# Optimization experiments

Hardware: AMD Instinct MI355X
Metric: run time of the kernel (lower is better)

Reference implementation:

```python
import jax, jax.numpy as jnp
import numpy as np

N = 100000
E = 3200000
H_MLP = 30   # EdgeMLP hidden dim
H_GCN = 10   # GCNEvaluator hidden dim
D_IN = 6     # node_dim + token_dim


def setup_inputs() -> dict:
    key = jax.random.key(0)
    ks = jax.random.split(key, 24)
    s = 0.1
    inp = {
        "x": jax.random.normal(ks[0], (N, 1), jnp.float32),
        "token": jax.random.normal(ks[1], (N, 5), jnp.float32),
        "edge_attr_gen": jax.random.normal(ks[2], (E, 1), jnp.float32),
        "edge_attr_eval": jax.random.uniform(ks[3], (E, 2), jnp.float32),
        "gumbel": jax.random.gumbel(ks[4], (E, 2), jnp.float32),
        "edge_index": jax.random.randint(ks[5], (2, E), 0, N, jnp.int32),
        # EdgeMLP params: Linear(13,30), Linear(30,30), Linear(30,30), Linear(30,2)
        "W0": jax.random.normal(ks[6], (2 * D_IN + 1, H_MLP), jnp.float32) * s,
        "b0": jnp.zeros((H_MLP,), jnp.float32),
        "W1": jax.random.normal(ks[7], (H_MLP, H_MLP), jnp.float32) * s,
        "b1": jnp.zeros((H_MLP,), jnp.float32),
        "W2": jax.random.normal(ks[8], (H_MLP, H_MLP), jnp.float32) * s,
        "b2": jnp.zeros((H_MLP,), jnp.float32),
        "W3": jax.random.normal(ks[9], (H_MLP, 2), jnp.float32) * s,
        "b3": jnp.zeros((2,), jnp.float32),
        # GCNEvaluator params
        "Wl": jax.random.normal(ks[10], (1, 1), jnp.float32) * s,   # edge_weight_lin
        "bl": jnp.zeros((1,), jnp.float32),
        "Wc": jax.random.normal(ks[11], (D_IN, H_GCN), jnp.float32) * s,  # GCNConv weight
        "bc": jnp.zeros((H_GCN,), jnp.float32),
        "Wo": jax.random.normal(ks[12], (H_GCN, 1), jnp.float32) * s,     # output Linear
        "bo": jnp.zeros((1,), jnp.float32),
    }
    return inp


def reference(x, token, edge_attr_gen, edge_attr_eval, gumbel, edge_index,
              W0, b0, W1, b1, W2, b2, W3, b3, Wl, bl, Wc, bc, Wo, bo):
    src = edge_index[0]
    tgt = edge_index[1]
    x_all = jnp.concatenate([x, token], axis=-1)              # [N, 6]

    # ---- generate_graph: edge gather + concat + MLP ----
    ef = jnp.concatenate([x_all[src], x_all[tgt], edge_attr_gen], axis=-1)  # [E, 13]
    h = jax.nn.relu(ef @ W0 + b0)
    h = jax.nn.relu(h @ W1 + b1)
    h = jax.nn.relu(h @ W2 + b2)
    logits = h @ W3 + b3                                      # [E, 2]

    # gumbel_softmax(tau=1.0, hard=True) with straight-through
    y_soft = jax.nn.softmax(logits + gumbel, axis=-1)
    y_hard = jax.nn.one_hot(jnp.argmax(y_soft, axis=-1), 2, dtype=y_soft.dtype)
    y = y_hard + y_soft - jax.lax.stop_gradient(y_soft)
    edge_value = y[:, 1:2]                                    # [E, 1]

    # ---- evaluate_graph: GCNEvaluator ----
    combined = jnp.concatenate([edge_attr_eval, edge_value], axis=-1)  # [E, 3]
    mask = combined[:, -2] * (1.0 - combined[:, -1])
    ew = jax.nn.sigmoid((combined[:, :1] @ Wl + bl)[:, 0]) * mask      # [E]

    # GCNConv(add_self_loops=True, normalize=True)
    loop = jnp.arange(N, dtype=src.dtype)
    row = jnp.concatenate([src, loop])
    col = jnp.concatenate([tgt, loop])
    w = jnp.concatenate([ew, jnp.ones((N,), ew.dtype)])
    deg = jax.ops.segment_sum(w, col, num_segments=N)
    dis = jnp.where(deg > 0, jax.lax.rsqrt(jnp.where(deg > 0, deg, 1.0)), 0.0)
    norm = dis[row] * w * dis[col]
    xw = x_all @ Wc                                            # [N, 10]
    agg = jax.ops.segment_sum(norm[:, None] * xw[row], col, num_segments=N) + bc
    out = jax.nn.sigmoid(agg @ Wo + bo)                        # [N, 1]
    return out
```

## Files before the change

kernel.cpp:

```cpp
#include <hip/hip_runtime.h>

#define NN 100000
#define NE 3200000
#define HM 30
#define HG 10
#define MAXK 26
#define OVF_CAP 8192

__global__ __launch_bounds__(256) void pack_kernel(
    const float* __restrict__ x, const float* __restrict__ token,
    const float* __restrict__ Wc,
    float* __restrict__ xall8, float* __restrict__ xwp)
{
    int n = blockIdx.x * 256 + threadIdx.x;
    if (n >= NN) return;

    float xa[6];
    xa[0] = x[n];
    #pragma unroll
    for (int i = 0; i < 5; i++) xa[1 + i] = token[n * 5 + i];

    float4* x4 = (float4*)xall8;
    x4[n * 2 + 0] = make_float4(xa[0], xa[1], xa[2], xa[3]);
    x4[n * 2 + 1] = make_float4(xa[4], xa[5], 0.f, 0.f);

    float w[12];
    #pragma unroll
    for (int k = 0; k < HG; k++) {
        float a = 0.f;
        #pragma unroll
        for (int i = 0; i < 6; i++) a = fmaf(xa[i], Wc[i * HG + k], a);
        w[k] = a;
    }
    w[10] = 0.f; w[11] = 0.f;
    float4* wp = (float4*)(xwp + (size_t)n * 12);
    wp[0] = make_float4(w[0], w[1], w[2], w[3]);
    wp[1] = make_float4(w[4], w[5], w[6], w[7]);
    wp[2] = make_float4(w[8], w[9], w[10], w[11]);
}

__global__ __launch_bounds__(256) void edge_mlp4_kernel(
    const float* __restrict__ xall8,
    const float* __restrict__ eg, const float* __restrict__ ee,
    const float* __restrict__ gum, const int* __restrict__ eidx,
    const float* __restrict__ W0, const float* __restrict__ b0,
    const float* __restrict__ W1, const float* __restrict__ b1,
    const float* __restrict__ W2, const float* __restrict__ b2,
    const float* __restrict__ W3, const float* __restrict__ b3,
    const float* __restrict__ Wl, const float* __restrict__ bl,
    float* __restrict__ slots_w, int* __restrict__ slots_s,
    int* __restrict__ cnt,
    int* __restrict__ ohead, int* __restrict__ onxt,
    float* __restrict__ ovf_w, int* __restrict__ ovf_s, int* __restrict__ novf)
{
    __shared__ float2 sW0p[15 * 13];
    __shared__ float2 sW1p[15 * 30];
    __shared__ float2 sW2p[15 * 30];
    __shared__ float2 sW3[HM];
    __shared__ float2 sb0p[15], sb1p[15], sb2p[15];
    __shared__ float sb3[2], sWl, sbl;

    for (int idx = threadIdx.x; idx < 15 * 13; idx += 256) {
        int jp = idx / 13, i = idx - jp * 13;
        sW0p[idx] = make_float2(W0[i * HM + 2 * jp], W0[i * HM + 2 * jp + 1]);
    }
    for (int idx = threadIdx.x; idx < 15 * 30; idx += 256) {
        int jp = idx / 30, i = idx - jp * 30;
        sW1p[idx] = make_float2(W1[i * HM + 2 * jp], W1[i * HM + 2 * jp + 1]);
        sW2p[idx] = make_float2(W2[i * HM + 2 * jp], W2[i * HM + 2 * jp + 1]);
    }
    if (threadIdx.x < HM) sW3[threadIdx.x] = ((const float2*)W3)[threadIdx.x];
    if (threadIdx.x < 15) {
        int j = threadIdx.x;
        sb0p[j] = make_float2(b0[2 * j], b0[2 * j + 1]);
        sb1p[j] = make_float2(b1[2 * j], b1[2 * j + 1]);
        sb2p[j] = make_float2(b2[2 * j], b2[2 * j + 1]);
    }
    if (threadIdx.x == 0) { sb3[0] = b3[0]; sb3[1] = b3[1]; sWl = Wl[0]; sbl = bl[0]; }
    __syncthreads();

    int e = blockIdx.x * 256 + threadIdx.x;
    int s = eidx[e];
    int t = eidx[NE + e];

    const float4* x4 = (const float4*)xall8;
    float4 qa = x4[s * 2], qb = x4[s * 2 + 1];
    float4 qc = x4[t * 2], qd = x4[t * 2 + 1];
    float ef[13] = { qa.x, qa.y, qa.z, qa.w, qb.x, qb.y,
                     qc.x, qc.y, qc.z, qc.w, qd.x, qd.y, eg[e] };

    float h[HM], h2[HM];
    #pragma unroll
    for (int jp = 0; jp < 15; jp++) {
        float a0 = sb0p[jp].x, a1 = sb0p[jp].y;
        #pragma unroll
        for (int i = 0; i < 13; i++) {
            float2 w = sW0p[jp * 13 + i];
            a0 = fmaf(ef[i], w.x, a0);
            a1 = fmaf(ef[i], w.y, a1);
        }
        h[2 * jp] = fmaxf(a0, 0.f);
        h[2 * jp + 1] = fmaxf(a1, 0.f);
    }
    #pragma unroll
    for (int jp = 0; jp < 15; jp++) {
        float a0 = sb1p[jp].x, a1 = sb1p[jp].y;
        #pragma unroll
        for (int i = 0; i < HM; i++) {
            float2 w = sW1p[jp * 30 + i];
            a0 = fmaf(h[i], w.x, a0);
            a1 = fmaf(h[i], w.y, a1);
        }
        h2[2 * jp] = fmaxf(a0, 0.f);
        h2[2 * jp + 1] = fmaxf(a1, 0.f);
    }
    #pragma unroll
    for (int jp = 0; jp < 15; jp++) {
        float a0 = sb2p[jp].x, a1 = sb2p[jp].y;
        #pragma unroll
        for (int i = 0; i < HM; i++) {
            float2 w = sW2p[jp * 30 + i];
            a0 = fmaf(h2[i], w.x, a0);
            a1 = fmaf(h2[i], w.y, a1);
        }
        h[2 * jp] = fmaxf(a0, 0.f);
        h[2 * jp + 1] = fmaxf(a1, 0.f);
    }
    float l0 = sb3[0], l1 = sb3[1];
    #pragma unroll
    for (int i = 0; i < HM; i++) {
        float2 w = sW3[i];
        l0 = fmaf(h[i], w.x, l0);
        l1 = fmaf(h[i], w.y, l1);
    }

    const float2 g2 = ((const float2*)gum)[e];
    float v0 = l0 + g2.x;
    float v1 = l1 + g2.y;

    float ew = 0.f;
    if (!(v1 > v0)) {
        const float2 e2 = ((const float2*)ee)[e];
        float z = fmaf(e2.x, sWl, sbl);
        ew = e2.y / (1.f + __expf(-z));
    }
    if (ew != 0.f) {
        int slot = atomicAdd(&cnt[t], 1);
        if (slot < MAXK) {
            size_t p = (size_t)t * MAXK + slot;
            slots_w[p] = ew;
            slots_s[p] = s;
        } else {
            int i = atomicAdd(novf, 1);
            if (i < OVF_CAP) {
                ovf_w[i] = ew;
                ovf_s[i] = s;
                onxt[i] = atomicExch(&ohead[t], i);
            }
        }
    }
}

__global__ __launch_bounds__(256) void node_deg_kernel(
    const float* __restrict__ slots_w, const int* __restrict__ cnt,
    const int* __restrict__ ohead, const int* __restrict__ onxt,
    const float* __restrict__ ovf_w,
    float* __restrict__ xwp, float* __restrict__ dis)
{
    int n = blockIdx.x * 256 + threadIdx.x;
    if (n >= NN) return;

    int c = cnt[n];
    int cc = c < MAXK ? c : MAXK;
    float deg = 0.f;
    for (int j = 0; j < cc; j++) deg += slots_w[(size_t)n * MAXK + j];
    for (int i = ohead[n]; i >= 0; i = onxt[i]) deg += ovf_w[i];

    float d = rsqrtf(deg + 1.0f);
    dis[n] = d;

    float4* wp = (float4*)(xwp + (size_t)n * 12);
    #pragma unroll
    for (int q = 0; q < 3; q++) {
        float4 v = wp[q];
        v.x *= d; v.y *= d; v.z *= d; v.w *= d;
        wp[q] = v;
    }
}

__global__ __launch_bounds__(256) void gather_out2_kernel(
    const float* __restrict__ slots_w, const int* __restrict__ slots_s,
    const int* __restrict__ cnt,
    const int* __restrict__ ohead, const int* __restrict__ onxt,
    const float* __restrict__ ovf_w, const int* __restrict__ ovf_s,
    const float* __restrict__ z, const float* __restrict__ dis,
    const float* __restrict__ bc, const float* __restrict__ Wo,
    const float* __restrict__ bo, float* __restrict__ out)
{
    int n = blockIdx.x * 256 + threadIdx.x;
    if (n >= NN) return;

    const float4* Z = (const float4*)z;
    float4 A0 = make_float4(0.f, 0.f, 0.f, 0.f), A1 = A0, A2 = A0;

    int c = cnt[n];
    int cc = c < MAXK ? c : MAXK;
    for (int j = 0; j < cc; j++) {
        size_t p = (size_t)n * MAXK + j;
        float w = slots_w[p];
        int s = slots_s[p];
        float4 z0 = Z[s * 3], z1 = Z[s * 3 + 1], z2 = Z[s * 3 + 2];
        A0.x = fmaf(w, z0.x, A0.x); A0.y = fmaf(w, z0.y, A0.y);
        A0.z = fmaf(w, z0.z, A0.z); A0.w = fmaf(w, z0.w, A0.w);
        A1.x = fmaf(w, z1.x, A1.x); A1.y = fmaf(w, z1.y, A1.y);
        A1.z = fmaf(w, z1.z, A1.z); A1.w = fmaf(w, z1.w, A1.w);
        A2.x = fmaf(w, z2.x, A2.x); A2.y = fmaf(w, z2.y, A2.y);
    }
    for (int i = ohead[n]; i >= 0; i = onxt[i]) {
        float w = ovf_w[i];
        int s = ovf_s[i];
        float4 z0 = Z[s * 3], z1 = Z[s * 3 + 1], z2 = Z[s * 3 + 2];
        A0.x = fmaf(w, z0.x, A0.x); A0.y = fmaf(w, z0.y, A0.y);
        A0.z = fmaf(w, z0.z, A0.z); A0.w = fmaf(w, z0.w, A0.w);
        A1.x = fmaf(w, z1.x, A1.x); A1.y = fmaf(w, z1.y, A1.y);
        A1.z = fmaf(w, z1.z, A1.z); A1.w = fmaf(w, z1.w, A1.w);
        A2.x = fmaf(w, z2.x, A2.x); A2.y = fmaf(w, z2.y, A2.y);
    }

    float4 s0 = Z[n * 3], s1 = Z[n * 3 + 1], s2 = Z[n * 3 + 2];
    A0.x += s0.x; A0.y += s0.y; A0.z += s0.z; A0.w += s0.w;
    A1.x += s1.x; A1.y += s1.y; A1.z += s1.z; A1.w += s1.w;
    A2.x += s2.x; A2.y += s2.y;

    float d = dis[n];
    float v[10] = { A0.x, A0.y, A0.z, A0.w, A1.x, A1.y, A1.z, A1.w, A2.x, A2.y };
    float o = bo[0];
    #pragma unroll
    for (int k = 0; k < HG; k++)
        o = fmaf(fmaf(v[k], d, bc[k]), Wo[k], o);
    out[n] = 1.f / (1.f + __expf(-o));
}

__global__ __launch_bounds__(256) void edge_mlp_kernel(
    const float* __restrict__ x, const float* __restrict__ token,
    const float* __restrict__ eg, const float* __restrict__ ee,
    const float* __restrict__ gum, const int* __restrict__ eidx,
    const float* __restrict__ W0, const float* __restrict__ b0,
    const float* __restrict__ W1, const float* __restrict__ b1,
    const float* __restrict__ W2, const float* __restrict__ b2,
    const float* __restrict__ W3, const float* __restrict__ b3,
    const float* __restrict__ Wl, const float* __restrict__ bl,
    float* __restrict__ ew_out, float* __restrict__ deg)
{
    int e = blockIdx.x * 256 + threadIdx.x;
    if (e >= NE) return;
    int s = eidx[e];
    int t = eidx[NE + e];

    float ef[13];
    ef[0] = x[s];
    #pragma unroll
    for (int i = 0; i < 5; i++) ef[1 + i] = token[s * 5 + i];
    ef[6] = x[t];
    #pragma unroll
    for (int i = 0; i < 5; i++) ef[7 + i] = token[t * 5 + i];
    ef[12] = eg[e];

    float h[HM], h2[HM];
    #pragma unroll
    for (int j = 0; j < HM; j++) {
        float a = b0[j];
        #pragma unroll
        for (int i = 0; i < 13; i++) a = fmaf(ef[i], W0[i * HM + j], a);
        h[j] = fmaxf(a, 0.f);
    }
    #pragma unroll
    for (int j = 0; j < HM; j++) {
        float a = b1[j];
        #pragma unroll
        for (int i = 0; i < HM; i++) a = fmaf(h[i], W1[i * HM + j], a);
        h2[j] = fmaxf(a, 0.f);
    }
    #pragma unroll
    for (int j = 0; j < HM; j++) {
        float a = b2[j];
        #pragma unroll
        for (int i = 0; i < HM; i++) a = fmaf(h2[i], W2[i * HM + j], a);
        h[j] = fmaxf(a, 0.f);
    }
    float l0 = b3[0], l1 = b3[1];
    #pragma unroll
    for (int i = 0; i < HM; i++) {
        l0 = fmaf(h[i], W3[i * 2 + 0], l0);
        l1 = fmaf(h[i], W3[i * 2 + 1], l1);
    }
    const float2 g2 = ((const float2*)gum)[e];
    float v0 = l0 + g2.x, v1 = l1 + g2.y;
    float ew = 0.f;
    if (!(v1 > v0)) {
        const float2 ee2 = ((const float2*)ee)[e];
        float z = fmaf(ee2.x, Wl[0], bl[0]);
        ew = ee2.y / (1.f + __expf(-z));
    }
    ew_out[e] = ew;
    if (ew != 0.f) atomicAdd(&deg[t], ew);
}

__global__ __launch_bounds__(256) void node_pre_kernel(
    const float* __restrict__ x, const float* __restrict__ token,
    const float* __restrict__ Wc, const float* __restrict__ deg,
    float* __restrict__ xw, float* __restrict__ dis)
{
    int n = blockIdx.x * 256 + threadIdx.x;
    if (n >= NN) return;
    float xa[6];
    xa[0] = x[n];
    #pragma unroll
    for (int i = 0; i < 5; i++) xa[1 + i] = token[n * 5 + i];
    #pragma unroll
    for (int k = 0; k < HG; k++) {
        float a = 0.f;
        #pragma unroll
        for (int i = 0; i < 6; i++) a = fmaf(xa[i], Wc[i * HG + k], a);
        xw[n * HG + k] = a;
    }
    dis[n] = rsqrtf(deg[n] + 1.0f);
}

__global__ __launch_bounds__(256) void edge_scatter_kernel(
    const int* __restrict__ eidx, const float* __restrict__ ew,
    const float* __restrict__ dis, const float* __restrict__ xw,
    float* __restrict__ agg)
{
    int e = blockIdx.x * 256 + threadIdx.x;
    if (e >= NE) return;
    float w = ew[e];
    if (w == 0.f) return;
    int s = eidx[e];
    int t = eidx[NE + e];
    float norm = dis[s] * w * dis[t];
    #pragma unroll
    for (int k = 0; k < HG; k++)
        atomicAdd(&agg[t * HG + k], norm * xw[s * HG + k]);
}

__global__ __launch_bounds__(256) void node_out_kernel(
    const float* __restrict__ agg, const float* __restrict__ xw,
    const float* __restrict__ dis, const float* __restrict__ bc,
    const float* __restrict__ Wo, const float* __restrict__ bo,
    float* __restrict__ out)
{
    int n = blockIdx.x * 256 + threadIdx.x;
    if (n >= NN) return;
    float d = dis[n];
    float self = d * d;
    float acc = bo[0];
    #pragma unroll
    for (int k = 0; k < HG; k++) {
        float v = agg[n * HG + k] + xw[n * HG + k] * self + bc[k];
        acc = fmaf(v, Wo[k], acc);
    }
    out[n] = 1.f / (1.f + __expf(-acc));
}

extern "C" void kernel_launch(void* const* d_in, const int* in_sizes, int n_in,
                              void* d_out, int out_size, void* d_ws, size_t ws_size,
                              hipStream_t stream) {
    const float* x   = (const float*)d_in[0];
    const float* tok = (const float*)d_in[1];
    const float* eg  = (const float*)d_in[2];
    const float* ee  = (const float*)d_in[3];
    const float* gum = (const float*)d_in[4];
    const int*   ei  = (const int*)d_in[5];
    const float* W0  = (const float*)d_in[6];
    const float* b0  = (const float*)d_in[7];
    const float* W1  = (const float*)d_in[8];
    const float* b1  = (const float*)d_in[9];
    const float* W2  = (const float*)d_in[10];
    const float* b2  = (const float*)d_in[11];
    const float* W3  = (const float*)d_in[12];
    const float* b3  = (const float*)d_in[13];
    const float* Wl  = (const float*)d_in[14];
    const float* bl  = (const float*)d_in[15];
    const float* Wc  = (const float*)d_in[16];
    const float* bc  = (const float*)d_in[17];
    const float* Wo  = (const float*)d_in[18];
    const float* bo  = (const float*)d_in[19];
    float* out = (float*)d_out;

    dim3 blk(256);
    dim3 egrid(NE / 256);
    dim3 ngrid((NN + 255) / 256);

    size_t off_xall8 = 0;
    size_t off_z     = off_xall8 + (size_t)NN * 8;
    size_t off_sw    = off_z + (size_t)NN * 12;
    size_t off_ss    = off_sw + (size_t)NN * MAXK;
    size_t off_cnt   = off_ss + (size_t)NN * MAXK;
    size_t off_novf  = off_cnt + NN;
    size_t off_dis   = off_novf + 1;
    size_t off_ohead = off_dis + NN;
    size_t off_ovfw  = off_ohead + NN;
    size_t off_ovfs  = off_ovfw + OVF_CAP;
    size_t off_onxt  = off_ovfs + OVF_CAP;
    size_t need_new  = (off_onxt + OVF_CAP) * sizeof(float);

    if (ws_size >= need_new) {
        float*  ws      = (float*)d_ws;
        float*  xall8   = ws + off_xall8;
        float*  z       = ws + off_z;
        float*  slots_w = ws + off_sw;
        int*    slots_s = (int*)(ws + off_ss);
        int*    cnt     = (int*)(ws + off_cnt);
        int*    novf    = (int*)(ws + off_novf);
        float*  dis     = ws + off_dis;
        int*    ohead   = (int*)(ws + off_ohead);
        float*  ovf_w   = ws + off_ovfw;
        int*    ovf_s   = (int*)(ws + off_ovfs);
        int*    onxt    = (int*)(ws + off_onxt);

        hipMemsetAsync(cnt, 0, (size_t)(NN + 1) * sizeof(int), stream);
        hipMemsetAsync(ohead, 0xFF, (size_t)NN * sizeof(int), stream);

        pack_kernel<<<ngrid, blk, 0, stream>>>(x, tok, Wc, xall8, z);
        edge_mlp4_kernel<<<egrid, blk, 0, stream>>>(xall8, eg, ee, gum, ei,
                                                    W0, b0, W1, b1, W2, b2, W3, b3,
                                                    Wl, bl, slots_w, slots_s, cnt,
                                                    ohead, onxt, ovf_w, ovf_s, novf);
        node_deg_kernel<<<ngrid, blk, 0, stream>>>(slots_w, cnt, ohead, onxt, ovf_w,
                                                   z, dis);
        gather_out2_kernel<<<ngrid, blk, 0, stream>>>(slots_w, slots_s, cnt,
                                                      ohead, onxt, ovf_w, ovf_s,
                                                      z, dis, bc, Wo, bo, out);
    } else {
        float* ws  = (float*)d_ws;
        float* ew  = ws;
        float* deg = ew + NE;
        float* agg = deg + NN;
        float* xw  = agg + (size_t)NN * HG;
        float* dis = xw + (size_t)NN * HG;

        hipMemsetAsync(deg, 0, (size_t)(NN + (size_t)NN * HG) * sizeof(float), stream);
        edge_mlp_kernel<<<egrid, blk, 0, stream>>>(x, tok, eg, ee, gum, ei,
                                                   W0, b0, W1, b1, W2, b2, W3, b3,
                                                   Wl, bl, ew, deg);
        node_pre_kernel<<<ngrid, blk, 0, stream>>>(x, tok, Wc, deg, xw, dis);
        edge_scatter_kernel<<<egrid, blk, 0, stream>>>(ei, ew, dis, xw, agg);
        node_out_kernel<<<ngrid, blk, 0, stream>>>(agg, xw, dis, bc, Wo, bo, out);
    }
}
```

Before: 455.6 us.

## Run edge MLP on bf16 MFMA with fp32 recheck of near-tie edges

Replaces the per-thread fp32 FMA edge MLP with wavefront-level bf16 MFMA (16x16x32) tiles, one wave handling 16 edges and passing activations between layers through LDS. Edges whose gumbel-argmax margin lies within a small tolerance are queued and recomputed in fp32 by a second kernel so that the hard selection matches the reference. This cuts the dominant MLP arithmetic cost but adds an extra launch and atomics. It also risks wrong results if the near-tie queue overflows its fixed capacity or if the bf16 error exceeds the tolerance.

```diff
diff --git a/kernel.cpp b/kernel.cpp
--- a/kernel.cpp
+++ b/kernel.cpp
@@ -6,6 +6,13 @@
 #define HG 10
 #define MAXK 26
 #define OVF_CAP 8192
+#define RCAP 65536
+#define TAU 0.01f
+
+typedef __bf16 bf16x8 __attribute__((ext_vector_type(8)));
+typedef float floatx4 __attribute__((ext_vector_type(4)));
+
+#define LDS_SYNC() asm volatile("s_waitcnt lgkmcnt(0)" ::: "memory")
 
 __global__ __launch_bounds__(256) void pack_kernel(
     const float* __restrict__ x, const float* __restrict__ token,
@@ -39,7 +46,7 @@
     wp[2] = make_float4(w[8], w[9], w[10], w[11]);
 }
 
-__global__ __launch_bounds__(256) void edge_mlp4_kernel(
+__global__ __launch_bounds__(256) void edge_mfma_kernel(
     const float* __restrict__ xall8,
     const float* __restrict__ eg, const float* __restrict__ ee,
     const float* __restrict__ gum, const int* __restrict__ eidx,
@@ -51,7 +58,164 @@
     float* __restrict__ slots_w, int* __restrict__ slots_s,
     int* __restrict__ cnt,
     int* __restrict__ ohead, int* __restrict__ onxt,
-    float* __restrict__ ovf_w, int* __restrict__ ovf_s, int* __restrict__ novf)
+    float* __restrict__ ovf_w, int* __restrict__ ovf_s, int* __restrict__ novf,
+    int* __restrict__ rid, int* __restrict__ ncheck)
+{
+    __shared__ __bf16 sT[4][16][40];
+    __shared__ float  sL[4][16][2];
+
+    const int tid  = threadIdx.x;
+    const int w    = tid >> 6;
+    const int lane = tid & 63;
+    const int quad = lane >> 4;
+    const int r    = lane & 15;
+    const int base = blockIdx.x * 64 + w * 16;
+
+    bf16x8 B0a, B0b, B1a, B1b, B2a, B2b, B3f;
+    {
+        const int c0 = r, c1 = 16 + r;
+        #pragma unroll
+        for (int j = 0; j < 8; j++) {
+            int k = quad * 8 + j;
+            B0a[j] = (k < 13)            ? (__bf16)W0[k * HM + c0] : (__bf16)0.f;
+            B0b[j] = (k < 13 && c1 < HM) ? (__bf16)W0[k * HM + c1] : (__bf16)0.f;
+            B1a[j] = (k < HM)            ? (__bf16)W1[k * HM + c0] : (__bf16)0.f;
+            B1b[j] = (k < HM && c1 < HM) ? (__bf16)W1[k * HM + c1] : (__bf16)0.f;
+            B2a[j] = (k < HM)            ? (__bf16)W2[k * HM + c0] : (__bf16)0.f;
+            B2b[j] = (k < HM && c1 < HM) ? (__bf16)W2[k * HM + c1] : (__bf16)0.f;
+            B3f[j] = (k < HM && c0 < 2)  ? (__bf16)W3[k * 2 + c0]  : (__bf16)0.f;
+        }
+    }
+
+    int s = 0, t = 0;
+    bf16x8 a;
+    #pragma unroll
+    for (int j = 0; j < 8; j++) a[j] = (__bf16)0.f;
+    if (quad < 2) {
+        int e = base + r;
+        t = eidx[NE + e];
+        const float4* x4 = (const float4*)xall8;
+        if (quad == 0) {
+            s = eidx[e];
+            float4 qa = x4[s * 2], qb = x4[s * 2 + 1], qc = x4[t * 2];
+            a[0] = (__bf16)qa.x; a[1] = (__bf16)qa.y; a[2] = (__bf16)qa.z; a[3] = (__bf16)qa.w;
+            a[4] = (__bf16)qb.x; a[5] = (__bf16)qb.y; a[6] = (__bf16)qc.x; a[7] = (__bf16)qc.y;
+        } else {
+            float4 qc = x4[t * 2], qd = x4[t * 2 + 1];
+            float egv = eg[e];
+            a[0] = (__bf16)qc.z; a[1] = (__bf16)qc.w; a[2] = (__bf16)qd.x; a[3] = (__bf16)qd.y;
+            a[4] = (__bf16)egv;
+        }
+    }
+
+    const int c1 = 16 + r;
+
+    {
+        float bb0 = b0[r];
+        float bb1 = (c1 < HM) ? b0[c1] : 0.f;
+        floatx4 acc0 = {bb0, bb0, bb0, bb0};
+        floatx4 acc1 = {bb1, bb1, bb1, bb1};
+        acc0 = __builtin_amdgcn_mfma_f32_16x16x32_bf16(a, B0a, acc0, 0, 0, 0);
+        acc1 = __builtin_amdgcn_mfma_f32_16x16x32_bf16(a, B0b, acc1, 0, 0, 0);
+        #pragma unroll
+        for (int reg = 0; reg < 4; reg++) {
+            int row = quad * 4 + reg;
+            sT[w][row][r]      = (__bf16)fmaxf(acc0[reg], 0.f);
+            sT[w][row][16 + r] = (__bf16)fmaxf(acc1[reg], 0.f);
+        }
+        LDS_SYNC();
+        a = *(const bf16x8*)&sT[w][r][quad * 8];
+    }
+    {
+        float bb0 = b1[r];
+        float bb1 = (c1 < HM) ? b1[c1] : 0.f;
+        floatx4 acc0 = {bb0, bb0, bb0, bb0};
+        floatx4 acc1 = {bb1, bb1, bb1, bb1};
+        acc0 = __builtin_amdgcn_mfma_f32_16x16x32_bf16(a, B1a, acc0, 0, 0, 0);
+        acc1 = __builtin_amdgcn_mfma_f32_16x16x32_bf16(a, B1b, acc1, 0, 0, 0);
+        LDS_SYNC();
+        #pragma unroll
+        for (int reg = 0; reg < 4; reg++) {
+            int row = quad * 4 + reg;
+            sT[w][row][r]      = (__bf16)fmaxf(acc0[reg], 0.f);
+            sT[w][row][16 + r] = (__bf16)fmaxf(acc1[reg], 0.f);
+        }
+        LDS_SYNC();
+        a = *(const bf16x8*)&sT[w][r][quad * 8];
+    }
+    {
+        float bb0 = b2[r];
+        float bb1 = (c1 < HM) ? b2[c1] : 0.f;
+        floatx4 acc0 = {bb0, bb0, bb0, bb0};
+        floatx4 acc1 = {bb1, bb1, bb1, bb1};
+        acc0 = __builtin_amdgcn_mfma_f32_16x16x32_bf16(a, B2a, acc0, 0, 0, 0);
+        acc1 = __builtin_amdgcn_mfma_f32_16x16x32_bf16(a, B2b, acc1, 0, 0, 0);
+        LDS_SYNC();
+        #pragma unroll
+        for (int reg = 0; reg < 4; reg++) {
+            int row = quad * 4 + reg;
+            sT[w][row][r]      = (__bf16)fmaxf(acc0[reg], 0.f);
+            sT[w][row][16 + r] = (__bf16)fmaxf(acc1[reg], 0.f);
+        }
+        LDS_SYNC();
+        a = *(const bf16x8*)&sT[w][r][quad * 8];
+    }
+    {
+        float bb = (r < 2) ? b3[r] : 0.f;
+        floatx4 acc = {bb, bb, bb, bb};
+        acc = __builtin_amdgcn_mfma_f32_16x16x32_bf16(a, B3f, acc, 0, 0, 0);
+        if (r < 2) {
+            #pragma unroll
+            for (int reg = 0; reg < 4; reg++)
+                sL[w][quad * 4 + reg][r] = acc[reg];
+        }
+        LDS_SYNC();
+    }
+
+    if (quad == 0) {
+        int e = base + r;
+        float l0 = sL[w][r][0], l1 = sL[w][r][1];
+        const float2 g = ((const float2*)gum)[e];
+        float margin = (l0 + g.x) - (l1 + g.y);
+        if (margin > TAU) {
+            const float2 e2 = ((const float2*)ee)[e];
+            float z = fmaf(e2.x, Wl[0], bl[0]);
+            float ew = e2.y / (1.f + __expf(-z));
+            if (ew != 0.f) {
+                int slot = atomicAdd(&cnt[t], 1);
+                if (slot < MAXK) {
+                    size_t p = (size_t)t * MAXK + slot;
+                    slots_w[p] = ew;
+                    slots_s[p] = s;
+                } else {
+                    int i = atomicAdd(novf, 1);
+                    if (i < OVF_CAP) {
+                        ovf_w[i] = ew; ovf_s[i] = s;
+                        onxt[i] = atomicExch(&ohead[t], i);
+                    }
+                }
+            }
+        } else if (margin >= -TAU) {
+            int i = atomicAdd(ncheck, 1);
+            if (i < RCAP) rid[i] = e;
+        }
+    }
+}
+
+__global__ __launch_bounds__(256) void recheck_kernel(
+    const float* __restrict__ xall8,
+    const float* __restrict__ eg, const float* __restrict__ ee,
+    const float* __restrict__ gum, const int* __restrict__ eidx,
+    const float* __restrict__ W0, const float* __restrict__ b0,
+    const float* __restrict__ W1, const float* __restrict__ b1,
+    const float* __restrict__ W2, const float* __restrict__ b2,
+    const float* __restrict__ W3, const float* __restrict__ b3,
+    const float* __restrict__ Wl, const float* __restrict__ bl,
+    float* __restrict__ slots_w, int* __restrict__ slots_s,
+    int* __restrict__ cnt,
+    int* __restrict__ ohead, int* __restrict__ onxt,
+    float* __restrict__ ovf_w, int* __restrict__ ovf_s, int* __restrict__ novf,
+    const int* __restrict__ rid, const int* __restrict__ ncheck)
 {
     __shared__ float2 sW0p[15 * 13];
     __shared__ float2 sW1p[15 * 30];
@@ -79,7 +243,12 @@
     if (threadIdx.x == 0) { sb3[0] = b3[0]; sb3[1] = b3[1]; sWl = Wl[0]; sbl = bl[0]; }
     __syncthreads();
 
-    int e = blockIdx.x * 256 + threadIdx.x;
+    int i0 = blockIdx.x * 256 + threadIdx.x;
+    int nc = *ncheck;
+    if (nc > RCAP) nc = RCAP;
+    if (i0 >= nc) return;
+
+    int e = rid[i0];
     int s = eidx[e];
     int t = eidx[NE + e];
 
@@ -138,24 +307,22 @@
     float v0 = l0 + g2.x;
     float v1 = l1 + g2.y;
 
-    float ew = 0.f;
     if (!(v1 > v0)) {
         const float2 e2 = ((const float2*)ee)[e];
         float z = fmaf(e2.x, sWl, sbl);
-        ew = e2.y / (1.f + __expf(-z));
-    }
-    if (ew != 0.f) {
-        int slot = atomicAdd(&cnt[t], 1);
-        if (slot < MAXK) {
-            size_t p = (size_t)t * MAXK + slot;
-            slots_w[p] = ew;
-            slots_s[p] = s;
-        } else {
-            int i = atomicAdd(novf, 1);
-            if (i < OVF_CAP) {
-                ovf_w[i] = ew;
-                ovf_s[i] = s;
-                onxt[i] = atomicExch(&ohead[t], i);
+        float ew = e2.y / (1.f + __expf(-z));
+        if (ew != 0.f) {
+            int slot = atomicAdd(&cnt[t], 1);
+            if (slot < MAXK) {
+                size_t p = (size_t)t * MAXK + slot;
+                slots_w[p] = ew;
+                slots_s[p] = s;
+            } else {
+                int i = atomicAdd(novf, 1);
+                if (i < OVF_CAP) {
+                    ovf_w[i] = ew; ovf_s[i] = s;
+                    onxt[i] = atomicExch(&ohead[t], i);
+                }
             }
         }
     }
@@ -389,21 +556,25 @@
     float* out = (float*)d_out;
 
     dim3 blk(256);
+    dim3 mgrid(NE / 64);
+    dim3 rgrid(RCAP / 256);
     dim3 egrid(NE / 256);
     dim3 ngrid((NN + 255) / 256);
 
-    size_t off_xall8 = 0;
-    size_t off_z     = off_xall8 + (size_t)NN * 8;
-    size_t off_sw    = off_z + (size_t)NN * 12;
-    size_t off_ss    = off_sw + (size_t)NN * MAXK;
-    size_t off_cnt   = off_ss + (size_t)NN * MAXK;
-    size_t off_novf  = off_cnt + NN;
-    size_t off_dis   = off_novf + 1;
-    size_t off_ohead = off_dis + NN;
-    size_t off_ovfw  = off_ohead + NN;
-    size_t off_ovfs  = off_ovfw + OVF_CAP;
-    size_t off_onxt  = off_ovfs + OVF_CAP;
-    size_t need_new  = (off_onxt + OVF_CAP) * sizeof(float);
+    size_t off_xall8  = 0;
+    size_t off_z      = off_xall8 + (size_t)NN * 8;
+    size_t off_sw     = off_z + (size_t)NN * 12;
+    size_t off_ss     = off_sw + (size_t)NN * MAXK;
+    size_t off_cnt    = off_ss + (size_t)NN * MAXK;
+    size_t off_novf   = off_cnt + NN;
+    size_t off_ncheck = off_novf + 1;
+    size_t off_dis    = off_ncheck + 1;
+    size_t off_ohead  = off_dis + NN;
+    size_t off_ovfw   = off_ohead + NN;
+    size_t off_ovfs   = off_ovfw + OVF_CAP;
+    size_t off_onxt   = off_ovfs + OVF_CAP;
+    size_t off_rid    = off_onxt + OVF_CAP;
+    size_t need_new   = (off_rid + RCAP) * sizeof(float);
 
     if (ws_size >= need_new) {
         float*  ws      = (float*)d_ws;
@@ -413,20 +584,28 @@
         int*    slots_s = (int*)(ws + off_ss);
         int*    cnt     = (int*)(ws + off_cnt);
         int*    novf    = (int*)(ws + off_novf);
+        int*    ncheck  = (int*)(ws + off_ncheck);
         float*  dis     = ws + off_dis;
         int*    ohead   = (int*)(ws + off_ohead);
         float*  ovf_w   = ws + off_ovfw;
         int*    ovf_s   = (int*)(ws + off_ovfs);
         int*    onxt    = (int*)(ws + off_onxt);
-
-        hipMemsetAsync(cnt, 0, (size_t)(NN + 1) * sizeof(int), stream);
+        int*    rid     = (int*)(ws + off_rid);
+
+        hipMemsetAsync(cnt, 0, (size_t)(NN + 2) * sizeof(int), stream);
         hipMemsetAsync(ohead, 0xFF, (size_t)NN * sizeof(int), stream);
 
         pack_kernel<<<ngrid, blk, 0, stream>>>(x, tok, Wc, xall8, z);
-        edge_mlp4_kernel<<<egrid, blk, 0, stream>>>(xall8, eg, ee, gum, ei,
+        edge_mfma_kernel<<<mgrid, blk, 0, stream>>>(xall8, eg, ee, gum, ei,
                                                     W0, b0, W1, b1, W2, b2, W3, b3,
                                                     Wl, bl, slots_w, slots_s, cnt,
-                                                    ohead, onxt, ovf_w, ovf_s, novf);
+                                                    ohead, onxt, ovf_w, ovf_s, novf,
+                                                    rid, ncheck);
+        recheck_kernel<<<rgrid, blk, 0, stream>>>(xall8, eg, ee, gum, ei,
+                                                  W0, b0, W1, b1, W2, b2, W3, b3,
+                                                  Wl, bl, slots_w, slots_s, cnt,
+                                                  ohead, onxt, ovf_w, ovf_s, novf,
+                                                  rid, ncheck);
         node_deg_kernel<<<ngrid, blk, 0, stream>>>(slots_w, cnt, ohead, onxt, ovf_w,
                                                    z, dis);
         gather_out2_kernel<<<ngrid, blk, 0, stream>>>(slots_w, slots_s, cnt,
```

New measurement: 819.8 us. +79.9%, slower.
